# Performance work log

Measured on AMD Instinct MI355X. Metric: run time of the kernel, lower is better.

The kernel has to match this reference:

```python
import jax, jax.numpy as jnp
import numpy as np

B, S, D = 2, 2048, 2048
N_HEADS, N_KV_HEADS, HEAD_DIM = 16, 8, 128
N_REP = N_HEADS // N_KV_HEADS
EPS = 1e-6
SCALE = HEAD_DIM ** -0.5


def setup_inputs() -> dict:
    key = jax.random.key(0)
    ks = jax.random.split(key, 6)
    x = jax.random.normal(ks[0], (B, S, D), dtype=jnp.float32)
    # RoPE frequencies (Llama-style cis stored as interleaved [cos, sin])
    inv_freq = 1.0 / (1e6 ** (jnp.arange(0, HEAD_DIM, 2, dtype=jnp.float32) / HEAD_DIM))
    angles = jnp.arange(S, dtype=jnp.float32)[:, None] * inv_freq[None, :]  # [S, HEAD_DIM//2]
    freqs_cis = jnp.stack([jnp.cos(angles), jnp.sin(angles)], axis=-1)  # [S, HEAD_DIM//2, 2]
    wq = jax.random.normal(ks[1], (N_HEADS * HEAD_DIM, D), dtype=jnp.float32) * 0.02
    wk = jax.random.normal(ks[2], (N_KV_HEADS * HEAD_DIM, D), dtype=jnp.float32) * 0.02
    wv = jax.random.normal(ks[3], (N_KV_HEADS * HEAD_DIM, D), dtype=jnp.float32) * 0.02
    wo = jax.random.normal(ks[4], (D, N_HEADS * HEAD_DIM), dtype=jnp.float32) * 0.02
    q_norm_w = jnp.ones((HEAD_DIM,), dtype=jnp.float32)
    k_norm_w = jnp.ones((HEAD_DIM,), dtype=jnp.float32)
    return {"x": x, "freqs_cis": freqs_cis, "wq": wq, "wk": wk, "wv": wv,
            "wo": wo, "q_norm_w": q_norm_w, "k_norm_w": k_norm_w}


def _rmsnorm(t, w):
    var = jnp.mean(jnp.square(t), axis=-1, keepdims=True)
    return t * jax.lax.rsqrt(var + EPS) * w


def _apply_rope(t, cos, sin):
    # t: [B, S, H, HEAD_DIM]; cos/sin: [1, S, 1, HEAD_DIM//2]
    tp = t.reshape(*t.shape[:-1], HEAD_DIM // 2, 2)
    tr, ti = tp[..., 0], tp[..., 1]
    out = jnp.stack([tr * cos - ti * sin, tr * sin + ti * cos], axis=-1)
    return out.reshape(t.shape)


def reference(x, freqs_cis, wq, wk, wv, wo, q_norm_w, k_norm_w):
    bs, seqlen, _ = x.shape
    xq = (x @ wq.T).reshape(bs, seqlen, N_HEADS, HEAD_DIM)
    xk = (x @ wk.T).reshape(bs, seqlen, N_KV_HEADS, HEAD_DIM)
    xv = (x @ wv.T).reshape(bs, seqlen, N_KV_HEADS, HEAD_DIM)
    # per-head RMSNorm (Qwen3)
    xq = _rmsnorm(xq, q_norm_w)
    xk = _rmsnorm(xk, k_norm_w)
    # rotary embedding
    cos = freqs_cis[:seqlen, :, 0][None, :, None, :]
    sin = freqs_cis[:seqlen, :, 1][None, :, None, :]
    xq = _apply_rope(xq, cos, sin)
    xk = _apply_rope(xk, cos, sin)
    # GQA: repeat kv heads
    keys = jnp.repeat(xk, N_REP, axis=2)    # [B, S, N_HEADS, HEAD_DIM]
    values = jnp.repeat(xv, N_REP, axis=2)
    q = xq.transpose(0, 2, 1, 3)   # [B, H, S, D]
    k = keys.transpose(0, 2, 1, 3)
    v = values.transpose(0, 2, 1, 3)
    scores = jnp.einsum("bhqd,bhkd->bhqk", q, k) * SCALE
    causal = jnp.tril(jnp.ones((seqlen, seqlen), dtype=bool))
    scores = jnp.where(causal[None, None], scores, jnp.finfo(scores.dtype).min)
    attn = jax.nn.softmax(scores, axis=-1)
    out = jnp.einsum("bhqk,bhkd->bhqd", attn, v)
    out = out.transpose(0, 2, 1, 3).reshape(bs, seqlen, N_HEADS * HEAD_DIM)
    return out @ wo.T
```

## Files before the change

### kernel.cpp

```cpp
#include <hip/hip_runtime.h>

#define B_ 2
#define S_ 2048
#define D_ 2048
#define NH 16
#define NKV 8
#define HD 128
#define SCALE 0.08838834764831845f
#define CEXP 0.1275255f
#define RTHR 62.733f

typedef unsigned short u16;
typedef __attribute__((ext_vector_type(8))) short short8;
typedef __attribute__((ext_vector_type(4))) float f32x4;
typedef __attribute__((ext_vector_type(16))) float f32x16;
typedef __attribute__((ext_vector_type(4))) int i32x4;
typedef __attribute__((ext_vector_type(2))) int i32x2;

#define ASM_VMCNT(N) asm volatile("s_waitcnt vmcnt(" #N ")" ::: "memory")
#define SBAR do { __builtin_amdgcn_sched_barrier(0); __builtin_amdgcn_s_barrier(); __builtin_amdgcn_sched_barrier(0); } while (0)
#define LGKM0 do { asm volatile("s_waitcnt lgkmcnt(0)" ::: "memory"); __builtin_amdgcn_sched_barrier(0); } while (0)

__device__ __forceinline__ u16 f2b(float f) {
  union { float f; unsigned u; } c; c.f = f;
  unsigned u = c.u;
  return (u16)((u + 0x7fffu + ((u >> 16) & 1u)) >> 16);
}
__device__ __forceinline__ float b2f(u16 h) {
  union { unsigned u; float f; } c; c.u = ((unsigned)h) << 16;
  return c.f;
}
__device__ __forceinline__ float exp2f_fast(float x) {
  float r; asm("v_exp_f32 %0, %1" : "=v"(r) : "v"(x)); return r;
}
__device__ __forceinline__ int cvtpk(float a, float b) {
  int r; asm("v_cvt_pk_bf16_f32 %0, %1, %2" : "=v"(r) : "v"(a), "v"(b)); return r;
}
__device__ __forceinline__ void pl32swap(int& a, int& b) {
  asm volatile("v_permlane32_swap_b32 %0, %1" : "+v"(a), "+v"(b));
}

__device__ __forceinline__ void load_lds16(const u16* g, u16* l) {
  __builtin_amdgcn_global_load_lds(
      (const __attribute__((address_space(1))) unsigned int*)g,
      (__attribute__((address_space(3))) unsigned int*)l, 16, 0, 0);
}

__global__ __launch_bounds__(256) void cvt_all(const float* __restrict__ x,
                                               const float* __restrict__ wq,
                                               const float* __restrict__ wk,
                                               const float* __restrict__ wv,
                                               const float* __restrict__ wo,
                                               u16* __restrict__ xb,
                                               u16* __restrict__ wqkvb,
                                               u16* __restrict__ wob) {
  const int blk = blockIdx.x;
  const float* src; u16* dst; int base;
  if (blk < 8192)       { src = x;  dst = xb;                  base = blk; }
  else if (blk < 12288) { src = wq; dst = wqkvb;               base = blk - 8192; }
  else if (blk < 14336) { src = wk; dst = wqkvb + 2048 * 2048; base = blk - 12288; }
  else if (blk < 16384) { src = wv; dst = wqkvb + 3072 * 2048; base = blk - 14336; }
  else                  { src = wo; dst = wob;                 base = blk - 16384; }
  int i = base * 256 + threadIdx.x;
  float4 v = ((const float4*)src)[i];
  u16 o0 = f2b(v.x), o1 = f2b(v.y), o2 = f2b(v.z), o3 = f2b(v.w);
  unsigned long long packed = (unsigned long long)o0 | ((unsigned long long)o1 << 16) |
                              ((unsigned long long)o2 << 32) | ((unsigned long long)o3 << 48);
  ((unsigned long long*)dst)[i] = packed;
}

#define LDA4(dst, SRC, MI0) \
  { _Pragma("unroll") for (int i2 = 0; i2 < 4; ++i2) { \
      const int arow = wr * 128 + (MI0 + i2) * 16 + r; \
      dst[i2] = *(const short8*)&(SRC)[arow * 32 + ((hi ^ ((arow >> 1) & 3)) << 3)]; } }
#define LDB4(dst, SRC) \
  { _Pragma("unroll") for (int n2 = 0; n2 < 4; ++n2) { \
      const int brow = wc * 64 + n2 * 16 + r; \
      dst[n2] = *(const short8*)&(SRC)[brow * 32 + ((hi ^ ((brow >> 1) & 3)) << 3)]; } }
#define MFMA16(MI0, AF, BF) \
  { __builtin_amdgcn_s_setprio(1); \
    _Pragma("unroll") for (int i2 = 0; i2 < 4; ++i2) \
    _Pragma("unroll") for (int n2 = 0; n2 < 4; ++n2) \
      acc[MI0 + i2][n2] = __builtin_amdgcn_mfma_f32_16x16x32_bf16(AF[i2], BF[n2], acc[MI0 + i2][n2], 0, 0, 0); \
    __builtin_amdgcn_s_setprio(0); }

template<int OUTF32>
__global__ __launch_bounds__(512, 2) void gemm256(const u16* __restrict__ A, const u16* __restrict__ Bm,
                                                  void* __restrict__ Cv, int M, int N, int K, int nbn) {
  __shared__ __align__(16) u16 As[2][2][8192];
  __shared__ __align__(16) u16 Bs[2][2][8192];
  const int tid = threadIdx.x;
  const int wave = tid >> 6, lane = tid & 63;
  const int cpx = gridDim.x >> 3;
  const int L = (blockIdx.x & 7) * cpx + (blockIdx.x >> 3);
  const int bm = L / nbn, bn = L % nbn;
  const int wr = wave >> 2, wc = wave & 3;
  const int r = lane & 15, hi = lane >> 4;
  const int rowA0 = bm * 256, rowB0 = bn * 256;

  f32x4 acc[8][4];
#pragma unroll
  for (int mi = 0; mi < 8; ++mi)
#pragma unroll
    for (int ni = 0; ni < 4; ++ni) acc[mi][ni] = (f32x4){0.f, 0.f, 0.f, 0.f};

  auto stage_half = [&](const u16* G, int rowbase, u16* ldsb, int kcol) {
#pragma unroll
    for (int l = 0; l < 2; ++l) {
      const int p = wave * 2048 + l * 1024 + lane * 16;
      const int row = p >> 6, slot = (p >> 4) & 3;
      const int kg = slot ^ ((row >> 1) & 3);
      load_lds16(G + (size_t)(rowbase + row) * K + kcol + kg * 8,
                 ldsb + ((wave * 2048 + l * 1024) >> 1));
    }
  };

  stage_half(A,  rowA0, &As[0][0][0], 0);
  stage_half(Bm, rowB0, &Bs[0][0][0], 0);
  stage_half(A,  rowA0, &As[0][1][0], 32);
  stage_half(Bm, rowB0, &Bs[0][1][0], 32);
  ASM_VMCNT(4);
  __builtin_amdgcn_s_barrier();

  const int nk = K >> 6;
  for (int kt = 0; kt < nk; ++kt) {
    const int c = kt & 1, nb2 = c ^ 1;
    const int kn = (kt + 1) << 6;
    const bool hn = kt + 1 < nk;
    const u16* a0 = As[c][0]; const u16* b0 = Bs[c][0];
    const u16* a1 = As[c][1]; const u16* b1 = Bs[c][1];
    short8 af[4], bf[4];
    LDB4(bf, b0); LDA4(af, a0, 0);
    if (hn) stage_half(A, rowA0, &As[nb2][0][0], kn);
    SBAR; LGKM0;
    MFMA16(0, af, bf);
    SBAR;
    LDA4(af, a0, 4);
    if (hn) stage_half(Bm, rowB0, &Bs[nb2][0][0], kn);
    ASM_VMCNT(4);
    SBAR; LGKM0;
    MFMA16(4, af, bf);
    SBAR;
    LDB4(bf, b1); LDA4(af, a1, 0);
    if (hn) stage_half(A, rowA0, &As[nb2][1][0], kn + 32);
    SBAR; LGKM0;
    MFMA16(0, af, bf);
    SBAR;
    LDA4(af, a1, 4);
    if (hn) stage_half(Bm, rowB0, &Bs[nb2][1][0], kn + 32);
    ASM_VMCNT(4);
    SBAR; LGKM0;
    MFMA16(4, af, bf);
    SBAR;
  }

#pragma unroll
  for (int mi = 0; mi < 8; ++mi)
#pragma unroll
    for (int ni = 0; ni < 4; ++ni)
#pragma unroll
      for (int r2 = 0; r2 < 4; ++r2) {
        int grow = bm * 256 + wr * 128 + mi * 16 + hi * 4 + r2;
        int gcol = bn * 256 + wc * 64 + ni * 16 + r;
        if (OUTF32)
          ((float*)Cv)[(size_t)grow * N + gcol] = acc[mi][ni][r2];
        else
          ((u16*)Cv)[(size_t)grow * N + gcol] = f2b(acc[mi][ni][r2]);
      }
}

template<int OUTF32>
__global__ __launch_bounds__(256, 2) void gemm_bt2(const u16* __restrict__ A, const u16* __restrict__ Bm,
                                                   void* __restrict__ Cv, int M, int N, int K, int nbn) {
  __shared__ __align__(16) u16 As[2][128 * 64];
  __shared__ __align__(16) u16 Bs[2][128 * 64];
  const int tid = threadIdx.x;
  const int wave = tid >> 6, lane = tid & 63;
  const int nwg = gridDim.x, cpx = nwg >> 3;
  const int L = (blockIdx.x & 7) * cpx + (blockIdx.x >> 3);
  const int bm = L / nbn, bn = L % nbn;
  const int wr = wave >> 1, wc = wave & 1;
  const int r = lane & 15, hi = lane >> 4;

  f32x4 acc[4][4];
#pragma unroll
  for (int m = 0; m < 4; ++m)
#pragma unroll
    for (int n = 0; n < 4; ++n) acc[m][n] = (f32x4){0.f, 0.f, 0.f, 0.f};

  const int gslot = (lane & 7) ^ (lane >> 3);
  const int srow = lane >> 3;

  auto stage = [&](int buf, int k0) {
#pragma unroll
    for (int jj = 0; jj < 4; ++jj) {
      int j = wave * 4 + jj;
      int row = j * 8 + srow;
      load_lds16(A + (size_t)(bm * 128 + row) * K + k0 + gslot * 8, &As[buf][j * 512]);
      load_lds16(Bm + (size_t)(bn * 128 + row) * K + k0 + gslot * 8, &Bs[buf][j * 512]);
    }
  };

  const int nk = K >> 6;
  stage(0, 0);
  for (int kt = 0; kt < nk; ++kt) {
    if (kt + 1 < nk) {
      stage((kt + 1) & 1, (kt + 1) << 6);
      ASM_VMCNT(8);
    } else {
      ASM_VMCNT(0);
    }
    SBAR;
    const u16* as = As[kt & 1];
    const u16* bs = Bs[kt & 1];
#pragma unroll
    for (int kc = 0; kc < 2; ++kc) {
      short8 af[4], bfr[4];
#pragma unroll
      for (int m = 0; m < 4; ++m) {
        int row = wr * 64 + m * 16 + r;
        int slot = (hi + kc * 4) ^ (row & 7);
        af[m] = *(const short8*)&as[row * 64 + slot * 8];
      }
#pragma unroll
      for (int n = 0; n < 4; ++n) {
        int row = wc * 64 + n * 16 + r;
        int slot = (hi + kc * 4) ^ (row & 7);
        bfr[n] = *(const short8*)&bs[row * 64 + slot * 8];
      }
#pragma unroll
      for (int m = 0; m < 4; ++m)
#pragma unroll
        for (int n = 0; n < 4; ++n)
          acc[m][n] = __builtin_amdgcn_mfma_f32_16x16x32_bf16(af[m], bfr[n], acc[m][n], 0, 0, 0);
    }
    SBAR;
  }

#pragma unroll
  for (int m = 0; m < 4; ++m)
#pragma unroll
    for (int n = 0; n < 4; ++n)
#pragma unroll
      for (int r2 = 0; r2 < 4; ++r2) {
        int grow = bm * 128 + wr * 64 + m * 16 + hi * 4 + r2;
        int gcol = bn * 128 + wc * 64 + n * 16 + r;
        if (OUTF32)
          ((float*)Cv)[(size_t)grow * N + gcol] = acc[m][n][r2];
        else
          ((u16*)Cv)[(size_t)grow * N + gcol] = f2b(acc[m][n][r2]);
      }
}

__global__ __launch_bounds__(256) void rmsnorm_rope(const u16* __restrict__ qkv, const float* __restrict__ fc,
                                                    const float* __restrict__ qw, const float* __restrict__ kw,
                                                    u16* __restrict__ qr, u16* __restrict__ kr) {
  const int tid = threadIdx.x, wave = tid >> 6, lane = tid & 63;
  const int rowid = blockIdx.x * 4 + wave;
  const int token = rowid / 24;
  const int hh = rowid % 24;
  const int b = token >> 11, s = token & 2047;
  const bool isq = hh < 16;
  const int off = isq ? hh * 128 : 2048 + (hh - 16) * 128;
  const u16* src = qkv + (size_t)token * 4096 + off + lane * 2;
  unsigned pv = *(const unsigned*)src;
  float t0 = b2f((u16)(pv & 0xffffu));
  float t1 = b2f((u16)(pv >> 16));
  float ss = t0 * t0 + t1 * t1;
#pragma unroll
  for (int mm = 1; mm < 64; mm <<= 1) ss += __shfl_xor(ss, mm, 64);
  float rms = rsqrtf(ss * (1.0f / 128.0f) + 1e-6f);
  const float* nw = isq ? qw : kw;
  t0 *= rms * nw[lane * 2];
  t1 *= rms * nw[lane * 2 + 1];
  float c = fc[(s * 64 + lane) * 2], sn = fc[(s * 64 + lane) * 2 + 1];
  float o0 = t0 * c - t1 * sn;
  float o1 = t0 * sn + t1 * c;
  unsigned ov = (unsigned)f2b(o0) | ((unsigned)f2b(o1) << 16);
  if (isq)
    *(unsigned*)(qr + ((size_t)(b * 16 + hh) * 2048 + s) * 128 + lane * 2) = ov;
  else
    *(unsigned*)(kr + ((size_t)(b * 8 + hh - 16) * 2048 + s) * 128 + lane * 2) = ov;
}

__global__ __launch_bounds__(256) void v_transpose(const u16* __restrict__ qkv, u16* __restrict__ vt) {
  __shared__ __align__(16) u16 tile[64][136];
  const int blk = blockIdx.x;
  const int st = blk & 31, h = (blk >> 5) & 7, b = blk >> 8;
  const int s0 = st * 64, t = threadIdx.x;
#pragma unroll
  for (int p = 0; p < 4; ++p) {
    int row = p * 16 + (t >> 4), c8 = (t & 15) * 8;
    const u16* src = qkv + (size_t)(b * 2048 + s0 + row) * 4096 + 3072 + h * 128 + c8;
    *(short8*)&tile[row][c8] = *(const short8*)src;
  }
  __syncthreads();
  const int d = t >> 1, j0 = (t & 1) * 32;
  u16* dst = vt + ((size_t)(b * 8 + h) * 128 + d) * 2048 + s0 + j0;
#pragma unroll
  for (int j = 0; j < 32; j += 8) {
    short8 v;
#pragma unroll
    for (int u = 0; u < 8; ++u) v[u] = (short)tile[j0 + j + u][d];
    *(short8*)(dst + j) = v;
  }
}

__global__ __launch_bounds__(256, 2) void attn6(const u16* __restrict__ qr, const u16* __restrict__ kr,
                                                const u16* __restrict__ vt, u16* __restrict__ ao) {
  __shared__ __align__(16) u16 Ks[2][64 * 128];
  __shared__ __align__(16) u16 Vs[2][128 * 64];
  const int tid = threadIdx.x, wave = tid >> 6, lane = tid & 63;
  const int ql = lane & 31, lh = lane >> 5;

  const int blk = blockIdx.x;
  const int half = blk >> 8;
  const int xcd = blk & 7;
  const int idx = (blk >> 3) & 31;
  const int bh = xcd * 4 + (idx & 3);
  const int pp = idx >> 2;
  const int t = half ? pp : 15 - pp;
  const int b = bh >> 4, h = bh & 15, hkv = h >> 1;

  const u16* Q  = qr + (size_t)(b * 16 + h) * S_ * HD;
  const u16* Kg = kr + (size_t)(b * 8 + hkv) * S_ * HD;
  const u16* Vg = vt + (size_t)(b * 8 + hkv) * HD * S_;

  const int q0w = t * 128 + wave * 32;
  const int nsteps = 2 * (t + 1);

  short8 qf[8];
#pragma unroll
  for (int ki = 0; ki < 8; ++ki)
    qf[ki] = *(const short8*)(Q + (size_t)(q0w + ql) * HD + ki * 16 + lh * 8);

  f32x16 o[4];
#pragma unroll
  for (int dt = 0; dt < 4; ++dt) o[dt] = 0.f;
  float m = -1e30f, l = 0.f;

  auto stage = [&](int buf, int kv0) {
#pragma unroll
    for (int inst = 0; inst < 4; ++inst) {
      int pp2 = wave * 4096 + inst * 1024 + lane * 16;
      int row = pp2 >> 8;
      int colb = (pp2 & 255) ^ ((row & 7) << 4);
      load_lds16(Kg + (((size_t)(kv0 + row)) << 7) + (colb >> 1),
                 &Ks[buf][(wave * 4096 + inst * 1024) >> 1]);
    }
#pragma unroll
    for (int inst = 0; inst < 4; ++inst) {
      int pp2 = wave * 4096 + inst * 1024 + lane * 16;
      int d = pp2 >> 7;
      int colb = (pp2 & 127) ^ ((d & 7) << 4);
      load_lds16(Vg + (size_t)d * S_ + kv0 + (colb >> 1),
                 &Vs[buf][(wave * 4096 + inst * 1024) >> 1]);
    }
  };

  stage(0, 0);
  for (int i = 0; i < nsteps; ++i) {
    const int kv0 = i * 64;
    const u16* kb = Ks[i & 1];
    const u16* vb = Vs[i & 1];
    if (i + 1 < nsteps) {
      stage((i + 1) & 1, kv0 + 64);
      ASM_VMCNT(8);
    } else {
      ASM_VMCNT(0);
    }
    SBAR;

    if (kv0 < q0w + 32) {
      f32x16 sacc[2];
      sacc[0] = 0.f; sacc[1] = 0.f;
      __builtin_amdgcn_s_setprio(1);
#pragma unroll
      for (int ki = 0; ki < 8; ++ki) {
        const int off = ki * 32 + lh * 16;
#pragma unroll
        for (int kvt = 0; kvt < 2; ++kvt) {
          const int row = kvt * 32 + ql;
          short8 kf = *(const short8*)&kb[(row << 7) + ((off ^ ((row & 7) << 4)) >> 1)];
          sacc[kvt] = __builtin_amdgcn_mfma_f32_32x32x16_bf16(kf, qf[ki], sacc[kvt], 0, 0, 0);
        }
      }
      __builtin_amdgcn_s_setprio(0);
      const int q = q0w + ql;
      if (kv0 + 64 > q0w) {
#pragma unroll
        for (int kvt = 0; kvt < 2; ++kvt) {
          const int kvb = kv0 + kvt * 32 + 4 * lh;
#pragma unroll
          for (int reg = 0; reg < 16; ++reg) {
            const int kvr = kvb + (reg & 3) + 8 * (reg >> 2);
            sacc[kvt][reg] = (kvr > q) ? -1e30f : sacc[kvt][reg];
          }
        }
      }
      float mx = sacc[0][0];
#pragma unroll
      for (int kvt = 0; kvt < 2; ++kvt)
#pragma unroll
        for (int reg = 0; reg < 16; ++reg) mx = fmaxf(mx, sacc[kvt][reg]);
      mx = fmaxf(mx, __shfl_xor(mx, 32, 64));
      if (__any(mx > m + RTHR)) {
        float mn = fmaxf(m, mx);
        float sc = exp2f_fast((m - mn) * CEXP);
        l *= sc;
        m = mn;
#pragma unroll
        for (int dt = 0; dt < 4; ++dt)
#pragma unroll
          for (int reg = 0; reg < 16; ++reg) o[dt][reg] *= sc;
      }
      short8 pf[4];
      const float mc = m * CEXP;
      float ps = 0.f;
#pragma unroll
      for (int kvt = 0; kvt < 2; ++kvt) {
        float pv[16];
#pragma unroll
        for (int reg = 0; reg < 16; ++reg) {
          pv[reg] = exp2f_fast(__builtin_fmaf(sacc[kvt][reg], CEXP, -mc));
          ps += pv[reg];
        }
        int A0 = cvtpk(pv[0], pv[1]),  B0 = cvtpk(pv[2], pv[3]);
        int C0 = cvtpk(pv[4], pv[5]),  D0 = cvtpk(pv[6], pv[7]);
        int A1 = cvtpk(pv[8], pv[9]),  B1 = cvtpk(pv[10], pv[11]);
        int C1 = cvtpk(pv[12], pv[13]), D1 = cvtpk(pv[14], pv[15]);
        pl32swap(A0, C0);
        pl32swap(B0, D0);
        pl32swap(A1, C1);
        pl32swap(B1, D1);
        i32x4 w0 = (i32x4){A0, B0, C0, D0};
        i32x4 w1 = (i32x4){A1, B1, C1, D1};
        pf[kvt * 2]     = *(short8*)&w0;
        pf[kvt * 2 + 1] = *(short8*)&w1;
      }
      l += ps;
      __builtin_amdgcn_s_setprio(1);
#pragma unroll
      for (int kc = 0; kc < 4; ++kc) {
        const int off = kc * 32 + lh * 16;
#pragma unroll
        for (int dt = 0; dt < 4; ++dt) {
          const int d = dt * 32 + ql;
          short8 vf = *(const short8*)&vb[(d << 6) + ((off ^ ((d & 7) << 4)) >> 1)];
          o[dt] = __builtin_amdgcn_mfma_f32_32x32x16_bf16(vf, pf[kc], o[dt], 0, 0, 0);
        }
      }
      __builtin_amdgcn_s_setprio(0);
    }
    SBAR;
  }

  l += __shfl_xor(l, 32, 64);
  const float inv = 1.0f / l;
  const size_t rowoff = ((size_t)(b * 2048 + q0w + ql)) * 2048 + h * 128;
#pragma unroll
  for (int dt = 0; dt < 4; ++dt)
#pragma unroll
    for (int g = 0; g < 4; ++g) {
      const int d0 = dt * 32 + 8 * g + 4 * lh;
      int w0 = cvtpk(o[dt][4 * g] * inv, o[dt][4 * g + 1] * inv);
      int w1 = cvtpk(o[dt][4 * g + 2] * inv, o[dt][4 * g + 3] * inv);
      i32x2 pk = (i32x2){w0, w1};
      *(i32x2*)((u16*)ao + rowoff + d0) = pk;
    }
}

extern "C" void kernel_launch(void* const* d_in, const int* in_sizes, int n_in,
                              void* d_out, int out_size, void* d_ws, size_t ws_size,
                              hipStream_t stream) {
  const float* x = (const float*)d_in[0];
  const float* fc = (const float*)d_in[1];
  const float* wq = (const float*)d_in[2];
  const float* wk = (const float*)d_in[3];
  const float* wv = (const float*)d_in[4];
  const float* wo = (const float*)d_in[5];
  const float* qw = (const float*)d_in[6];
  const float* kw = (const float*)d_in[7];
  float* out = (float*)d_out;
  char* ws = (char*)d_ws;

  u16* xb    = (u16*)(ws);
  u16* wqkvb = (u16*)(ws + 16777216);
  u16* wob   = (u16*)(ws + 33554432);
  u16* qkv   = (u16*)(ws + 41943040);
  u16* qrope = (u16*)(ws + 75497472);
  u16* krope = (u16*)(ws + 92274688);
  u16* vtb   = (u16*)(ws + 100663296);
  u16* ao    = (u16*)(ws + 109051904);

  cvt_all<<<20480, 256, 0, stream>>>(x, wq, wk, wv, wo, xb, wqkvb, wob);

  gemm256<0><<<256, 512, 0, stream>>>(xb, wqkvb, (void*)qkv, 4096, 4096, 2048, 16);

  rmsnorm_rope<<<24576, 256, 0, stream>>>(qkv, fc, qw, kw, qrope, krope);
  v_transpose<<<512, 256, 0, stream>>>(qkv, vtb);

  attn6<<<512, 256, 0, stream>>>(qrope, krope, vtb, ao);

  gemm_bt2<1><<<512, 256, 0, stream>>>(ao, wob, (void*)out, 4096, 2048, 2048, 16);
}
```

Baseline: 212.8 us.

## Software-pipeline LDS fragment loads ahead of MFMAs in GEMM main loop

The GEMM k-loop now uses separate register sets for even/odd A fragments and two B fragments, so LDS reads for the next MFMA group are issued before the current MFMAs run. The explicit lgkmcnt(0) waits and half the barriers are dropped, and the vmcnt waits are reworked. The next iteration's first fragments are prefetched at the end of each iteration. This adds register pressure, and the correctness of the removed LDS waits and reordered staging depends on the compiler inserting the right waitcnts.

```diff
diff --git a/kernel.cpp b/kernel.cpp
--- a/kernel.cpp
+++ b/kernel.cpp
@@ -19,7 +19,6 @@
 
 #define ASM_VMCNT(N) asm volatile("s_waitcnt vmcnt(" #N ")" ::: "memory")
 #define SBAR do { __builtin_amdgcn_sched_barrier(0); __builtin_amdgcn_s_barrier(); __builtin_amdgcn_sched_barrier(0); } while (0)
-#define LGKM0 do { asm volatile("s_waitcnt lgkmcnt(0)" ::: "memory"); __builtin_amdgcn_sched_barrier(0); } while (0)
 
 __device__ __forceinline__ u16 f2b(float f) {
   union { float f; unsigned u; } c; c.f = f;
@@ -122,36 +121,37 @@
   ASM_VMCNT(4);
   __builtin_amdgcn_s_barrier();
 
+  short8 afE[4], afO[4], bf0[4], bf1[4];
+  LDA4(afE, As[0][0], 0);
+  LDB4(bf0, Bs[0][0]);
+
   const int nk = K >> 6;
   for (int kt = 0; kt < nk; ++kt) {
     const int c = kt & 1, nb2 = c ^ 1;
     const int kn = (kt + 1) << 6;
     const bool hn = kt + 1 < nk;
-    const u16* a0 = As[c][0]; const u16* b0 = Bs[c][0];
-    const u16* a1 = As[c][1]; const u16* b1 = Bs[c][1];
-    short8 af[4], bf[4];
-    LDB4(bf, b0); LDA4(af, a0, 0);
+    LDA4(afO, As[c][0], 4);
     if (hn) stage_half(A, rowA0, &As[nb2][0][0], kn);
-    SBAR; LGKM0;
-    MFMA16(0, af, bf);
-    SBAR;
-    LDA4(af, a0, 4);
+    SBAR;
+    MFMA16(0, afE, bf0);
+    if (hn) { ASM_VMCNT(2); } else { ASM_VMCNT(0); }
+    LDA4(afE, As[c][1], 0);
+    LDB4(bf1, Bs[c][1]);
     if (hn) stage_half(Bm, rowB0, &Bs[nb2][0][0], kn);
-    ASM_VMCNT(4);
-    SBAR; LGKM0;
-    MFMA16(4, af, bf);
-    SBAR;
-    LDB4(bf, b1); LDA4(af, a1, 0);
+    SBAR;
+    MFMA16(4, afO, bf0);
+    LDA4(afO, As[c][1], 4);
     if (hn) stage_half(A, rowA0, &As[nb2][1][0], kn + 32);
-    SBAR; LGKM0;
-    MFMA16(0, af, bf);
-    SBAR;
-    LDA4(af, a1, 4);
-    if (hn) stage_half(Bm, rowB0, &Bs[nb2][1][0], kn + 32);
-    ASM_VMCNT(4);
-    SBAR; LGKM0;
-    MFMA16(4, af, bf);
-    SBAR;
+    SBAR;
+    MFMA16(0, afE, bf1);
+    if (hn) {
+      ASM_VMCNT(2);
+      LDA4(afE, As[nb2][0], 0);
+      LDB4(bf0, Bs[nb2][0]);
+      stage_half(Bm, rowB0, &Bs[nb2][1][0], kn + 32);
+    }
+    SBAR;
+    MFMA16(4, afO, bf1);
   }
 
 #pragma unroll
```

Result: no change. 213.2 us (+0.2%).
